# Optimization experiments

Measured on AMD Instinct MI355X. Metric: run time of the kernel, lower is better.

## Reference

```python
import jax, jax.numpy as jnp
import numpy as np
from math import gamma, comb

D_POLY = 4
OFFSET = 2
EVAL_MAX = 1.4
N_NODES = 50000
N_EDGES = 800000
IN_FEATS = 256
H_FEATS = 64
NEG_SLOPE = 0.01  # F.leaky_relu / nn.LeakyReLU default


def _beta(a, b):
    return gamma(a) * gamma(b) / gamma(a + b)


def _calculate_theta2(d=D_POLY):
    # Closed-form expansion of sympy poly in calculate_theta2:
    # f(x) = (x/e)^i * (1 - x/e)^(d-i+offset) / (e * Beta(i+1, d+1-i+offset))
    # Returns ascending-order coefficient lists (theta[k] = coeff of x^k).
    e = EVAL_MAX
    thetas = []
    for i in range(OFFSET, d + 1 + OFFSET):
        m = d - i + OFFSET
        B = _beta(i + 1, d + 1 - i + OFFSET)
        c = np.zeros(d + 1 + OFFSET, dtype=np.float64)
        for j in range(m + 1):
            c[i + j] = (1.0 / e) ** i * comb(m, j) * (-1.0 / e) ** j / (e * B)
        thetas.append([float(v) for v in c])
    return thetas


THETAS = _calculate_theta2()


def setup_inputs() -> dict:
    key = jax.random.key(0)
    k1, k2, k3, k4, k5 = jax.random.split(key, 5)
    x = jax.random.normal(k1, (N_NODES, IN_FEATS), dtype=jnp.float32)
    W = jax.random.normal(k2, (IN_FEATS, H_FEATS), dtype=jnp.float32) * 0.05
    b = jax.random.normal(k3, (H_FEATS,), dtype=jnp.float32) * 0.05
    src = jax.random.randint(k4, (N_EDGES,), 0, N_NODES, dtype=jnp.int32)
    dst = jax.random.randint(k5, (N_EDGES,), 0, N_NODES, dtype=jnp.int32)
    return {"x": x, "W": W, "b": b, "src": src, "dst": dst}


def reference(x, W, b, src, dst):
    # BWGNN forward: linear + LeakyReLU, then 5 Beta-wavelet PolyConv filters.
    h = jax.nn.leaky_relu(x @ W + b, NEG_SLOPE)  # [N, H]
    # out_degrees, clamped to 1, then D^{-1/2}
    deg = jax.ops.segment_sum(jnp.ones_like(src, dtype=h.dtype), src, num_segments=N_NODES)
    d_inv = jnp.clip(deg, 1.0) ** -0.5
    d_inv = d_inv[:, None]  # [N, 1]
    outs = []
    for theta in THETAS:
        f = h
        acc = theta[0] * h
        for k in range(1, len(theta)):
            # unnLaplacian: f <- f - D^{-1/2} A^T D^{-1/2} f  (copy_u/sum SpMM)
            msg = jax.ops.segment_sum((f * d_inv)[src], dst, num_segments=N_NODES)
            f = f - msg * d_inv
            acc = acc + theta[k] * f
        outs.append(acc)
    return jnp.concatenate(outs, axis=1)  # [N, 5*H]
```

## Files before the change

### kernel.cpp

```cpp
#include <hip/hip_runtime.h>
#include <math.h>

#define NN 50000
#define NNH 25000
#define NE 800000
#define INF 256
#define HF 64
#define OUTF 320
#define NB ((NN + 255) / 256)
#define G 128
#define SL (NE / G)

typedef _Float16 half8 __attribute__((ext_vector_type(8)));
typedef float floatx4 __attribute__((ext_vector_type(4)));

static __device__ __forceinline__ unsigned short f2h(float x) {
    _Float16 h = (_Float16)x;
    return *(unsigned short*)&h;
}
static __device__ __forceinline__ float h2f(unsigned short u) {
    _Float16 h = *(_Float16*)&u;
    return (float)h;
}

struct ThetaM { float m[5][7]; };

static void compute_theta(ThetaM& tm) {
    const double e = 1.4;
    auto fact = [](int n) { double r = 1.0; for (int i = 2; i <= n; ++i) r *= i; return r; };
    for (int t = 0; t < 5; ++t) {
        int i = t + 2;
        int mm = 6 - i;
        double B = fact(i) * fact(6 - i) / fact(7);
        for (int k = 0; k < 7; ++k) tm.m[t][k] = 0.f;
        for (int j = 0; j <= mm; ++j) {
            double cb = fact(mm) / (fact(j) * fact(mm - j));
            double v = pow(1.0 / e, (double)i) * cb * pow(-1.0 / e, (double)j) / (e * B);
            tm.m[t][i + j] = (float)v;
        }
    }
}

__global__ __launch_bounds__(1024) void hist_kernel(const int* __restrict__ src,
                                                    const int* __restrict__ dst,
                                                    unsigned short* __restrict__ hist_src,
                                                    unsigned short* __restrict__ hist_dst) {
    __shared__ unsigned int h[NNH];
    int b = blockIdx.x;
    const int* arr = (b < G) ? dst : src;
    unsigned short* outp = (b < G) ? hist_dst : hist_src;
    int bb = (b < G) ? b : b - G;
    for (int i = threadIdx.x; i < NNH; i += 1024) h[i] = 0u;
    __syncthreads();
    int base = bb * SL;
    for (int i = threadIdx.x; i < SL; i += 1024) {
        int d = arr[base + i];
        atomicAdd(&h[d >> 1], 1u << ((d & 1) * 16));
    }
    __syncthreads();
    unsigned int* out32 = (unsigned int*)(outp + (size_t)bb * NN);
    for (int i = threadIdx.x; i < NNH; i += 1024) out32[i] = h[i];
}

__global__ __launch_bounds__(256) void merge_dst_kernel(unsigned short* __restrict__ hist,
                                                        int* __restrict__ cnt,
                                                        int* __restrict__ partial) {
    __shared__ int s[256];
    int tid = threadIdx.x;
    int d = blockIdx.x * 256 + tid;
    int run = 0;
    if (d < NN) {
        for (int b = 0; b < G; ++b) {
            size_t idx = (size_t)b * NN + d;
            int v = hist[idx];
            hist[idx] = (unsigned short)run;
            run += v;
        }
        cnt[d] = run;
    }
    s[tid] = run;
    __syncthreads();
    for (int off = 128; off > 0; off >>= 1) {
        if (tid < off) s[tid] += s[tid + off];
        __syncthreads();
    }
    if (tid == 0) partial[blockIdx.x] = s[0];
}

__global__ __launch_bounds__(256) void merge_src_kernel(const unsigned short* __restrict__ hist,
                                                        float* __restrict__ dinv) {
    int d = blockIdx.x * 256 + threadIdx.x;
    if (d >= NN) return;
    int run = 0;
    for (int b = 0; b < G; ++b) run += hist[(size_t)b * NN + d];
    float dd = (float)run;
    if (dd < 1.f) dd = 1.f;
    dinv[d] = 1.0f / sqrtf(dd);
}

__global__ __launch_bounds__(256) void scan_partials_kernel(const int* __restrict__ partial,
                                                            int* __restrict__ offsets,
                                                            int* __restrict__ row_ptr) {
    __shared__ int s[256];
    int tid = threadIdx.x;
    s[tid] = (tid < NB) ? partial[tid] : 0;
    __syncthreads();
    for (int off = 1; off < 256; off <<= 1) {
        int t = (tid >= off) ? s[tid - off] : 0;
        __syncthreads();
        s[tid] += t;
        __syncthreads();
    }
    if (tid < NB) offsets[tid] = (tid == 0) ? 0 : s[tid - 1];
    if (tid == 0) row_ptr[NN] = NE;
}

__global__ __launch_bounds__(256) void scan_write_kernel(const int* __restrict__ cnt,
                                                         const int* __restrict__ offsets,
                                                         int* __restrict__ row_ptr) {
    __shared__ int s[256];
    int tid = threadIdx.x;
    int gid = blockIdx.x * 256 + tid;
    int c = (gid < NN) ? cnt[gid] : 0;
    s[tid] = c;
    __syncthreads();
    for (int off = 1; off < 256; off <<= 1) {
        int t = (tid >= off) ? s[tid - off] : 0;
        __syncthreads();
        s[tid] += t;
        __syncthreads();
    }
    if (gid < NN) row_ptr[gid] = offsets[blockIdx.x] + s[tid] - c;
}

__global__ __launch_bounds__(1024) void fill_kernel(const int* __restrict__ src,
                                                    const int* __restrict__ dst,
                                                    const unsigned short* __restrict__ hist_dst,
                                                    const int* __restrict__ row_ptr,
                                                    int* __restrict__ col) {
    __shared__ unsigned int cur[NNH];
    int b = blockIdx.x;
    for (int i = threadIdx.x; i < NNH; i += 1024) cur[i] = 0u;
    __syncthreads();
    int base = b * SL;
    const unsigned short* hrow = hist_dst + (size_t)b * NN;
    for (int i = threadIdx.x; i < SL; i += 1024) {
        int d = dst[base + i];
        int sh = (d & 1) * 16;
        unsigned int old = atomicAdd(&cur[d >> 1], 1u << sh);
        int rank = (int)((old >> sh) & 0xFFFFu);
        int pos = row_ptr[d] + (int)hrow[d] + rank;
        col[pos] = src[base + i];
    }
}

__global__ __launch_bounds__(256) void wprep_kernel(const float* __restrict__ W,
                                                    unsigned short* __restrict__ Wt) {
    int id = blockIdx.x * 256 + threadIdx.x;
    if (id >= HF * INF) return;
    int n = id >> 8;
    int k = id & 255;
    Wt[id] = f2h(W[k * HF + n]);
}

__global__ __launch_bounds__(256) void gemm_kernel(const float* __restrict__ x,
                                                   const unsigned short* __restrict__ Wt,
                                                   const float* __restrict__ b,
                                                   const float* __restrict__ dinv,
                                                   float* __restrict__ f,
                                                   unsigned short* __restrict__ g) {
    __shared__ _Float16 wls[64 * 264];
    __shared__ _Float16 xls[64 * 136];
    int tid = threadIdx.x;
    int row0 = blockIdx.x * 64;
    int wave = tid >> 6;
    int lane = tid & 63;
    int q = lane >> 4;
    int ln = lane & 15;

    {
        const uint4* wg = (const uint4*)Wt;
        for (int i = 0; i < 8; ++i) {
            int l = tid + i * 256;
            int r = l >> 5, c = l & 31;
            *(uint4*)&wls[r * 264 + c * 8] = wg[l];
        }
    }

    floatx4 acc[4] = {{0.f,0.f,0.f,0.f},{0.f,0.f,0.f,0.f},{0.f,0.f,0.f,0.f},{0.f,0.f,0.f,0.f}};

    for (int ch = 0; ch < 2; ++ch) {
        __syncthreads();
        for (int i = 0; i < 8; ++i) {
            int l = tid + i * 256;
            int r = l >> 5, c4 = (l & 31) * 4;
            int grow = row0 + r;
            float4 v = make_float4(0.f, 0.f, 0.f, 0.f);
            if (grow < NN) v = *(const float4*)&x[(size_t)grow * INF + ch * 128 + c4];
            ushort4 hv;
            hv.x = f2h(v.x); hv.y = f2h(v.y); hv.z = f2h(v.z); hv.w = f2h(v.w);
            *(ushort4*)&xls[r * 136 + c4] = hv;
        }
        __syncthreads();
        int m = wave * 16 + ln;
        #pragma unroll
        for (int kb4 = 0; kb4 < 4; ++kb4) {
            int kb = kb4 * 32;
            half8 a = *(const half8*)&xls[m * 136 + kb + q * 8];
            int kg = ch * 128 + kb + q * 8;
            #pragma unroll
            for (int t = 0; t < 4; ++t) {
                half8 bb = *(const half8*)&wls[(t * 16 + ln) * 264 + kg];
                acc[t] = __builtin_amdgcn_mfma_f32_16x16x32_f16(a, bb, acc[t], 0, 0, 0);
            }
        }
    }

    float bias[4];
    #pragma unroll
    for (int t = 0; t < 4; ++t) bias[t] = b[t * 16 + ln];
    #pragma unroll
    for (int r = 0; r < 4; ++r) {
        int grow = row0 + wave * 16 + q * 4 + r;
        if (grow < NN) {
            float dv = dinv[grow];
            #pragma unroll
            for (int t = 0; t < 4; ++t) {
                float h = acc[t][r] + bias[t];
                h = (h > 0.f) ? h : 0.01f * h;
                int cidx = t * 16 + ln;
                f[(size_t)grow * HF + cidx] = h;
                g[(size_t)grow * HF + cidx] = f2h(h * dv);
            }
        }
    }
}

__global__ __launch_bounds__(256) void prop_kernel(const int* __restrict__ row_ptr,
                                                   const int* __restrict__ col,
                                                   const float* __restrict__ dinv,
                                                   const unsigned int* __restrict__ g_in,
                                                   const float* __restrict__ f_in, int fin_stride,
                                                   float* __restrict__ f_out, int fout_stride,
                                                   unsigned int* __restrict__ g_out) {
    int gidx = blockIdx.x * 256 + threadIdx.x;
    int wid = gidx >> 5;
    int c2 = threadIdx.x & 31;
    if (wid >= NN) return;
    int start = row_ptr[wid];
    int end   = row_ptr[wid + 1];
    float s0 = 0.f, s1 = 0.f;
    int j = start;
    for (; j + 8 <= end; j += 8) {
        unsigned int u0 = g_in[col[j + 0] * 32 + c2];
        unsigned int u1 = g_in[col[j + 1] * 32 + c2];
        unsigned int u2 = g_in[col[j + 2] * 32 + c2];
        unsigned int u3 = g_in[col[j + 3] * 32 + c2];
        unsigned int u4 = g_in[col[j + 4] * 32 + c2];
        unsigned int u5 = g_in[col[j + 5] * 32 + c2];
        unsigned int u6 = g_in[col[j + 6] * 32 + c2];
        unsigned int u7 = g_in[col[j + 7] * 32 + c2];
        s0 += ((h2f(u0 & 0xFFFF) + h2f(u1 & 0xFFFF)) + (h2f(u2 & 0xFFFF) + h2f(u3 & 0xFFFF)))
            + ((h2f(u4 & 0xFFFF) + h2f(u5 & 0xFFFF)) + (h2f(u6 & 0xFFFF) + h2f(u7 & 0xFFFF)));
        s1 += ((h2f(u0 >> 16) + h2f(u1 >> 16)) + (h2f(u2 >> 16) + h2f(u3 >> 16)))
            + ((h2f(u4 >> 16) + h2f(u5 >> 16)) + (h2f(u6 >> 16) + h2f(u7 >> 16)));
    }
    for (; j < end; ++j) {
        unsigned int u = g_in[col[j] * 32 + c2];
        s0 += h2f(u & 0xFFFF);
        s1 += h2f(u >> 16);
    }
    float dv = dinv[wid];
    float2 fv = *(const float2*)&f_in[(size_t)wid * fin_stride + 2 * c2];
    float fx = fv.x - s0 * dv;
    float fy = fv.y - s1 * dv;
    *(float2*)&f_out[(size_t)wid * fout_stride + 2 * c2] = make_float2(fx, fy);
    if (g_out) g_out[wid * 32 + c2] = (unsigned int)f2h(fx * dv) | ((unsigned int)f2h(fy * dv) << 16);
}

__global__ __launch_bounds__(256) void final_kernel(float* __restrict__ out, ThetaM tm) {
    int idx = blockIdx.x * 256 + threadIdx.x;
    if (idx >= NN * HF) return;
    int n = idx >> 6;
    int c = idx & 63;
    float v[5];
    #pragma unroll
    for (int j = 0; j < 5; ++j) v[j] = out[(size_t)n * OUTF + j * HF + c];
    #pragma unroll
    for (int t = 0; t < 5; ++t) {
        float o = 0.f;
        #pragma unroll
        for (int j = 0; j < 5; ++j) {
            if (j >= t) o += tm.m[t][j + 2] * v[j];
        }
        out[(size_t)n * OUTF + t * HF + c] = o;
    }
}

extern "C" void kernel_launch(void* const* d_in, const int* in_sizes, int n_in,
                              void* d_out, int out_size, void* d_ws, size_t ws_size,
                              hipStream_t stream) {
    const float* x  = (const float*)d_in[0];
    const float* W  = (const float*)d_in[1];
    const float* b  = (const float*)d_in[2];
    const int* src  = (const int*)d_in[3];
    const int* dst  = (const int*)d_in[4];
    float* out = (float*)d_out;

    char* ws = (char*)d_ws;
    size_t off = 0;
    auto alloc = [&](size_t bytes) -> void* {
        void* p = ws + off;
        off += (bytes + 255) & ~(size_t)255;
        return p;
    };
    unsigned short* hist_dst = (unsigned short*)alloc((size_t)G * NN * 2);
    unsigned short* hist_src = (unsigned short*)alloc((size_t)G * NN * 2);
    int*   cnt_dst = (int*)alloc((size_t)NN * 4);
    int*   row_ptr = (int*)alloc((size_t)(NN + 1) * 4);
    int*   partial = (int*)alloc((size_t)NB * 4);
    int*   offsets = (int*)alloc((size_t)NB * 4);
    float* dinv    = (float*)alloc((size_t)NN * 4);
    int*   col     = (int*)alloc((size_t)NE * 4);
    unsigned short* wt = (unsigned short*)alloc((size_t)HF * INF * 2);
    float* fbuf    = (float*)alloc((size_t)NN * HF * 4);
    unsigned short* gA = (unsigned short*)alloc((size_t)NN * HF * 2);
    unsigned short* gB = (unsigned short*)alloc((size_t)NN * HF * 2);

    hist_kernel<<<2 * G, 1024, 0, stream>>>(src, dst, hist_src, hist_dst);
    merge_dst_kernel<<<NB, 256, 0, stream>>>(hist_dst, cnt_dst, partial);
    merge_src_kernel<<<NB, 256, 0, stream>>>(hist_src, dinv);
    scan_partials_kernel<<<1, 256, 0, stream>>>(partial, offsets, row_ptr);
    scan_write_kernel<<<NB, 256, 0, stream>>>(cnt_dst, offsets, row_ptr);
    fill_kernel<<<G, 1024, 0, stream>>>(src, dst, hist_dst, row_ptr, col);
    wprep_kernel<<<(HF * INF + 255) / 256, 256, 0, stream>>>(W, wt);
    gemm_kernel<<<(NN + 63) / 64, 256, 0, stream>>>(x, wt, b, dinv, fbuf, gA);

    const int PB = (NN * 32 + 255) / 256;
    prop_kernel<<<PB, 256, 0, stream>>>(row_ptr, col, dinv, (unsigned int*)gA, fbuf, HF, fbuf, HF, (unsigned int*)gB);
    prop_kernel<<<PB, 256, 0, stream>>>(row_ptr, col, dinv, (unsigned int*)gB, fbuf, HF, out + 0 * HF, OUTF, (unsigned int*)gA);
    prop_kernel<<<PB, 256, 0, stream>>>(row_ptr, col, dinv, (unsigned int*)gA, out + 0 * HF, OUTF, out + 1 * HF, OUTF, (unsigned int*)gB);
    prop_kernel<<<PB, 256, 0, stream>>>(row_ptr, col, dinv, (unsigned int*)gB, out + 1 * HF, OUTF, out + 2 * HF, OUTF, (unsigned int*)gA);
    prop_kernel<<<PB, 256, 0, stream>>>(row_ptr, col, dinv, (unsigned int*)gA, out + 2 * HF, OUTF, out + 3 * HF, OUTF, (unsigned int*)gB);
    prop_kernel<<<PB, 256, 0, stream>>>(row_ptr, col, dinv, (unsigned int*)gB, out + 3 * HF, OUTF, out + 4 * HF, OUTF, nullptr);

    ThetaM tm;
    compute_theta(tm);
    final_kernel<<<(NN * HF + 255) / 256, 256, 0, stream>>>(out, tm);
}
```

Baseline: 346.2 us.

## Pad CSR rows to multiples of four, pack histograms into bytes, use atomic degrees

Destination histograms are packed as 8-bit counts, four nodes per word, which halves shared-memory and workspace traffic. Source degrees are now counted with global atomics instead of a second histogram pass, and the separate source-merge kernel is removed. Each CSR row is padded to a multiple of four with a dummy zero-feature node, so the propagation kernel can load column indices as int4 vectors and needs no scalar tail loop. Nontemporal loads and stores are added to streaming accesses, and the final theta-combine kernel is vectorized over pairs of features. The risks are 8-bit count overflow if any node receives more than 255 edges within one slice, and extra gathers for the padding entries.

```diff
diff --git a/kernel.cpp b/kernel.cpp
--- a/kernel.cpp
+++ b/kernel.cpp
@@ -2,17 +2,19 @@
 #include <math.h>
 
 #define NN 50000
-#define NNH 25000
+#define NN4 12500
 #define NE 800000
 #define INF 256
 #define HF 64
 #define OUTF 320
-#define NB ((NN + 255) / 256)
+#define NB4 ((NN4 + 255) / 256)
 #define G 128
 #define SL (NE / G)
 
 typedef _Float16 half8 __attribute__((ext_vector_type(8)));
 typedef float floatx4 __attribute__((ext_vector_type(4)));
+typedef float f32x2 __attribute__((ext_vector_type(2)));
+typedef float f32x4 __attribute__((ext_vector_type(4)));
 
 static __device__ __forceinline__ unsigned short f2h(float x) {
     _Float16 h = (_Float16)x;
@@ -41,61 +43,73 @@
     }
 }
 
-__global__ __launch_bounds__(1024) void hist_kernel(const int* __restrict__ src,
-                                                    const int* __restrict__ dst,
-                                                    unsigned short* __restrict__ hist_src,
-                                                    unsigned short* __restrict__ hist_dst) {
-    __shared__ unsigned int h[NNH];
+__global__ __launch_bounds__(1024) void zero_kernel(int* __restrict__ deg,
+                                                    unsigned int* __restrict__ gA,
+                                                    unsigned int* __restrict__ gB) {
+    int i = blockIdx.x * 1024 + threadIdx.x;
+    if (i < NN) deg[i] = 0;
+    if (blockIdx.x == 0 && threadIdx.x < 32) {
+        gA[NN * 32 + threadIdx.x] = 0u;
+        gB[NN * 32 + threadIdx.x] = 0u;
+    }
+}
+
+__global__ __launch_bounds__(1024) void histdeg_kernel(const int* __restrict__ src,
+                                                       const int* __restrict__ dst,
+                                                       unsigned int* __restrict__ hist,
+                                                       int* __restrict__ deg) {
+    __shared__ unsigned int h[NN4];
     int b = blockIdx.x;
-    const int* arr = (b < G) ? dst : src;
-    unsigned short* outp = (b < G) ? hist_dst : hist_src;
-    int bb = (b < G) ? b : b - G;
-    for (int i = threadIdx.x; i < NNH; i += 1024) h[i] = 0u;
-    __syncthreads();
-    int base = bb * SL;
+    for (int i = threadIdx.x; i < NN4; i += 1024) h[i] = 0u;
+    __syncthreads();
+    int base = b * SL;
     for (int i = threadIdx.x; i < SL; i += 1024) {
-        int d = arr[base + i];
-        atomicAdd(&h[d >> 1], 1u << ((d & 1) * 16));
-    }
-    __syncthreads();
-    unsigned int* out32 = (unsigned int*)(outp + (size_t)bb * NN);
-    for (int i = threadIdx.x; i < NNH; i += 1024) out32[i] = h[i];
-}
-
-__global__ __launch_bounds__(256) void merge_dst_kernel(unsigned short* __restrict__ hist,
+        int d = dst[base + i];
+        atomicAdd(&h[d >> 2], 1u << ((d & 3) * 8));
+    }
+    for (int i = threadIdx.x; i < SL; i += 1024) {
+        atomicAdd(&deg[src[base + i]], 1);
+    }
+    __syncthreads();
+    unsigned int* out32 = hist + (size_t)b * NN4;
+    for (int i = threadIdx.x; i < NN4; i += 1024) out32[i] = h[i];
+}
+
+__global__ __launch_bounds__(256) void merge_dst_kernel(unsigned int* __restrict__ hist,
+                                                        const int* __restrict__ deg,
                                                         int* __restrict__ cnt,
+                                                        float* __restrict__ dinv,
                                                         int* __restrict__ partial) {
     __shared__ int s[256];
     int tid = threadIdx.x;
-    int d = blockIdx.x * 256 + tid;
-    int run = 0;
-    if (d < NN) {
+    int t = blockIdx.x * 256 + tid;
+    int run0 = 0, run1 = 0, run2 = 0, run3 = 0;
+    if (t < NN4) {
         for (int b = 0; b < G; ++b) {
-            size_t idx = (size_t)b * NN + d;
-            int v = hist[idx];
-            hist[idx] = (unsigned short)run;
-            run += v;
-        }
-        cnt[d] = run;
-    }
-    s[tid] = run;
+            size_t idx = (size_t)b * NN4 + t;
+            unsigned int u = hist[idx];
+            hist[idx] = (unsigned int)run0 | ((unsigned int)run1 << 8) |
+                        ((unsigned int)run2 << 16) | ((unsigned int)run3 << 24);
+            run0 += u & 255u; run1 += (u >> 8) & 255u;
+            run2 += (u >> 16) & 255u; run3 += u >> 24;
+        }
+        *(int4*)&cnt[4 * t] = make_int4(run0, run1, run2, run3);
+        int4 dg = *(const int4*)&deg[4 * t];
+        float d0 = (float)(dg.x < 1 ? 1 : dg.x);
+        float d1 = (float)(dg.y < 1 ? 1 : dg.y);
+        float d2 = (float)(dg.z < 1 ? 1 : dg.z);
+        float d3 = (float)(dg.w < 1 ? 1 : dg.w);
+        *(float4*)&dinv[4 * t] = make_float4(1.0f / sqrtf(d0), 1.0f / sqrtf(d1),
+                                             1.0f / sqrtf(d2), 1.0f / sqrtf(d3));
+    }
+    int pad = ((run0 + 3) & ~3) + ((run1 + 3) & ~3) + ((run2 + 3) & ~3) + ((run3 + 3) & ~3);
+    s[tid] = pad;
     __syncthreads();
     for (int off = 128; off > 0; off >>= 1) {
         if (tid < off) s[tid] += s[tid + off];
         __syncthreads();
     }
     if (tid == 0) partial[blockIdx.x] = s[0];
-}
-
-__global__ __launch_bounds__(256) void merge_src_kernel(const unsigned short* __restrict__ hist,
-                                                        float* __restrict__ dinv) {
-    int d = blockIdx.x * 256 + threadIdx.x;
-    if (d >= NN) return;
-    int run = 0;
-    for (int b = 0; b < G; ++b) run += hist[(size_t)b * NN + d];
-    float dd = (float)run;
-    if (dd < 1.f) dd = 1.f;
-    dinv[d] = 1.0f / sqrtf(dd);
 }
 
 __global__ __launch_bounds__(256) void scan_partials_kernel(const int* __restrict__ partial,
@@ -103,7 +117,7 @@
                                                             int* __restrict__ row_ptr) {
     __shared__ int s[256];
     int tid = threadIdx.x;
-    s[tid] = (tid < NB) ? partial[tid] : 0;
+    s[tid] = (tid < NB4) ? partial[tid] : 0;
     __syncthreads();
     for (int off = 1; off < 256; off <<= 1) {
         int t = (tid >= off) ? s[tid - off] : 0;
@@ -111,44 +125,56 @@
         s[tid] += t;
         __syncthreads();
     }
-    if (tid < NB) offsets[tid] = (tid == 0) ? 0 : s[tid - 1];
-    if (tid == 0) row_ptr[NN] = NE;
+    if (tid < NB4) offsets[tid] = (tid == 0) ? 0 : s[tid - 1];
+    if (tid == NB4 - 1) row_ptr[NN] = s[tid];
 }
 
 __global__ __launch_bounds__(256) void scan_write_kernel(const int* __restrict__ cnt,
                                                          const int* __restrict__ offsets,
-                                                         int* __restrict__ row_ptr) {
+                                                         int* __restrict__ row_ptr,
+                                                         int* __restrict__ col) {
     __shared__ int s[256];
     int tid = threadIdx.x;
-    int gid = blockIdx.x * 256 + tid;
-    int c = (gid < NN) ? cnt[gid] : 0;
-    s[tid] = c;
+    int t = blockIdx.x * 256 + tid;
+    int4 c = make_int4(0, 0, 0, 0);
+    if (t < NN4) c = *(const int4*)&cnt[4 * t];
+    int p0 = (c.x + 3) & ~3, p1 = (c.y + 3) & ~3, p2 = (c.z + 3) & ~3, p3 = (c.w + 3) & ~3;
+    int csum = p0 + p1 + p2 + p3;
+    s[tid] = csum;
     __syncthreads();
     for (int off = 1; off < 256; off <<= 1) {
-        int t = (tid >= off) ? s[tid - off] : 0;
-        __syncthreads();
-        s[tid] += t;
-        __syncthreads();
-    }
-    if (gid < NN) row_ptr[gid] = offsets[blockIdx.x] + s[tid] - c;
+        int v = (tid >= off) ? s[tid - off] : 0;
+        __syncthreads();
+        s[tid] += v;
+        __syncthreads();
+    }
+    if (t < NN4) {
+        int b0 = offsets[blockIdx.x] + s[tid] - csum;
+        int b1 = b0 + p0, b2 = b1 + p1, b3 = b2 + p2;
+        *(int4*)&row_ptr[4 * t] = make_int4(b0, b1, b2, b3);
+        for (int k = c.x; k < p0; ++k) col[b0 + k] = NN;
+        for (int k = c.y; k < p1; ++k) col[b1 + k] = NN;
+        for (int k = c.z; k < p2; ++k) col[b2 + k] = NN;
+        for (int k = c.w; k < p3; ++k) col[b3 + k] = NN;
+    }
 }
 
 __global__ __launch_bounds__(1024) void fill_kernel(const int* __restrict__ src,
                                                     const int* __restrict__ dst,
-                                                    const unsigned short* __restrict__ hist_dst,
+                                                    const unsigned char* __restrict__ hist8,
                                                     const int* __restrict__ row_ptr,
                                                     int* __restrict__ col) {
-    __shared__ unsigned int cur[NNH];
+    __shared__ unsigned int cur[NN4];
     int b = blockIdx.x;
-    for (int i = threadIdx.x; i < NNH; i += 1024) cur[i] = 0u;
+    for (int i = threadIdx.x; i < NN4; i += 1024) cur[i] = 0u;
     __syncthreads();
     int base = b * SL;
-    const unsigned short* hrow = hist_dst + (size_t)b * NN;
+    const unsigned char* hrow = hist8 + (size_t)b * NN;
     for (int i = threadIdx.x; i < SL; i += 1024) {
         int d = dst[base + i];
-        int sh = (d & 1) * 16;
-        unsigned int old = atomicAdd(&cur[d >> 1], 1u << sh);
-        int rank = (int)((old >> sh) & 0xFFFFu);
+        int sh = (d & 3) * 8;
+        unsigned int old = atomicAdd(&cur[d >> 2], 1u << sh);
+        int rank = (int)((old >> sh) & 255u);
         int pos = row_ptr[d] + (int)hrow[d] + rank;
         col[pos] = src[base + i];
     }
@@ -195,10 +221,10 @@
             int l = tid + i * 256;
             int r = l >> 5, c4 = (l & 31) * 4;
             int grow = row0 + r;
-            float4 v = make_float4(0.f, 0.f, 0.f, 0.f);
-            if (grow < NN) v = *(const float4*)&x[(size_t)grow * INF + ch * 128 + c4];
+            f32x4 v = {0.f, 0.f, 0.f, 0.f};
+            if (grow < NN) v = __builtin_nontemporal_load((const f32x4*)&x[(size_t)grow * INF + ch * 128 + c4]);
             ushort4 hv;
-            hv.x = f2h(v.x); hv.y = f2h(v.y); hv.z = f2h(v.z); hv.w = f2h(v.w);
+            hv.x = f2h(v[0]); hv.y = f2h(v[1]); hv.z = f2h(v[2]); hv.w = f2h(v[3]);
             *(ushort4*)&xls[r * 136 + c4] = hv;
         }
         __syncthreads();
@@ -247,53 +273,60 @@
     int wid = gidx >> 5;
     int c2 = threadIdx.x & 31;
     if (wid >= NN) return;
-    int start = row_ptr[wid];
-    int end   = row_ptr[wid + 1];
+    int j   = row_ptr[wid];
+    int end = row_ptr[wid + 1];
     float s0 = 0.f, s1 = 0.f;
-    int j = start;
     for (; j + 8 <= end; j += 8) {
-        unsigned int u0 = g_in[col[j + 0] * 32 + c2];
-        unsigned int u1 = g_in[col[j + 1] * 32 + c2];
-        unsigned int u2 = g_in[col[j + 2] * 32 + c2];
-        unsigned int u3 = g_in[col[j + 3] * 32 + c2];
-        unsigned int u4 = g_in[col[j + 4] * 32 + c2];
-        unsigned int u5 = g_in[col[j + 5] * 32 + c2];
-        unsigned int u6 = g_in[col[j + 6] * 32 + c2];
-        unsigned int u7 = g_in[col[j + 7] * 32 + c2];
+        int4 ca = *(const int4*)&col[j];
+        int4 cb = *(const int4*)&col[j + 4];
+        unsigned int u0 = g_in[ca.x * 32 + c2];
+        unsigned int u1 = g_in[ca.y * 32 + c2];
+        unsigned int u2 = g_in[ca.z * 32 + c2];
+        unsigned int u3 = g_in[ca.w * 32 + c2];
+        unsigned int u4 = g_in[cb.x * 32 + c2];
+        unsigned int u5 = g_in[cb.y * 32 + c2];
+        unsigned int u6 = g_in[cb.z * 32 + c2];
+        unsigned int u7 = g_in[cb.w * 32 + c2];
         s0 += ((h2f(u0 & 0xFFFF) + h2f(u1 & 0xFFFF)) + (h2f(u2 & 0xFFFF) + h2f(u3 & 0xFFFF)))
             + ((h2f(u4 & 0xFFFF) + h2f(u5 & 0xFFFF)) + (h2f(u6 & 0xFFFF) + h2f(u7 & 0xFFFF)));
         s1 += ((h2f(u0 >> 16) + h2f(u1 >> 16)) + (h2f(u2 >> 16) + h2f(u3 >> 16)))
             + ((h2f(u4 >> 16) + h2f(u5 >> 16)) + (h2f(u6 >> 16) + h2f(u7 >> 16)));
     }
-    for (; j < end; ++j) {
-        unsigned int u = g_in[col[j] * 32 + c2];
-        s0 += h2f(u & 0xFFFF);
-        s1 += h2f(u >> 16);
+    if (j < end) {
+        int4 ca = *(const int4*)&col[j];
+        unsigned int u0 = g_in[ca.x * 32 + c2];
+        unsigned int u1 = g_in[ca.y * 32 + c2];
+        unsigned int u2 = g_in[ca.z * 32 + c2];
+        unsigned int u3 = g_in[ca.w * 32 + c2];
+        s0 += (h2f(u0 & 0xFFFF) + h2f(u1 & 0xFFFF)) + (h2f(u2 & 0xFFFF) + h2f(u3 & 0xFFFF));
+        s1 += (h2f(u0 >> 16) + h2f(u1 >> 16)) + (h2f(u2 >> 16) + h2f(u3 >> 16));
     }
     float dv = dinv[wid];
-    float2 fv = *(const float2*)&f_in[(size_t)wid * fin_stride + 2 * c2];
-    float fx = fv.x - s0 * dv;
-    float fy = fv.y - s1 * dv;
-    *(float2*)&f_out[(size_t)wid * fout_stride + 2 * c2] = make_float2(fx, fy);
+    f32x2 fv = __builtin_nontemporal_load((const f32x2*)&f_in[(size_t)wid * fin_stride + 2 * c2]);
+    float fx = fv[0] - s0 * dv;
+    float fy = fv[1] - s1 * dv;
+    f32x2 ov; ov[0] = fx; ov[1] = fy;
+    __builtin_nontemporal_store(ov, (f32x2*)&f_out[(size_t)wid * fout_stride + 2 * c2]);
     if (g_out) g_out[wid * 32 + c2] = (unsigned int)f2h(fx * dv) | ((unsigned int)f2h(fy * dv) << 16);
 }
 
 __global__ __launch_bounds__(256) void final_kernel(float* __restrict__ out, ThetaM tm) {
     int idx = blockIdx.x * 256 + threadIdx.x;
-    if (idx >= NN * HF) return;
-    int n = idx >> 6;
-    int c = idx & 63;
-    float v[5];
+    if (idx >= NN * 32) return;
+    int n = idx >> 5;
+    int c = (idx & 31) * 2;
+    f32x2 v[5];
     #pragma unroll
-    for (int j = 0; j < 5; ++j) v[j] = out[(size_t)n * OUTF + j * HF + c];
+    for (int j = 0; j < 5; ++j)
+        v[j] = __builtin_nontemporal_load((const f32x2*)&out[(size_t)n * OUTF + j * HF + c]);
     #pragma unroll
     for (int t = 0; t < 5; ++t) {
-        float o = 0.f;
+        f32x2 o = {0.f, 0.f};
         #pragma unroll
         for (int j = 0; j < 5; ++j) {
-            if (j >= t) o += tm.m[t][j + 2] * v[j];
-        }
-        out[(size_t)n * OUTF + t * HF + c] = o;
+            if (j >= t) { o[0] += tm.m[t][j + 2] * v[j][0]; o[1] += tm.m[t][j + 2] * v[j][1]; }
+        }
+        __builtin_nontemporal_store(o, (f32x2*)&out[(size_t)n * OUTF + t * HF + c]);
     }
 }
 
@@ -314,25 +347,25 @@
         off += (bytes + 255) & ~(size_t)255;
         return p;
     };
-    unsigned short* hist_dst = (unsigned short*)alloc((size_t)G * NN * 2);
-    unsigned short* hist_src = (unsigned short*)alloc((size_t)G * NN * 2);
-    int*   cnt_dst = (int*)alloc((size_t)NN * 4);
+    unsigned int* hist_dst = (unsigned int*)alloc((size_t)G * NN4 * 4);
+    int*   deg     = (int*)alloc((size_t)NN * 4);
+    int*   cnt     = (int*)alloc((size_t)NN * 4);
     int*   row_ptr = (int*)alloc((size_t)(NN + 1) * 4);
-    int*   partial = (int*)alloc((size_t)NB * 4);
-    int*   offsets = (int*)alloc((size_t)NB * 4);
+    int*   partial = (int*)alloc((size_t)NB4 * 4);
+    int*   offsets = (int*)alloc((size_t)NB4 * 4);
     float* dinv    = (float*)alloc((size_t)NN * 4);
-    int*   col     = (int*)alloc((size_t)NE * 4);
+    int*   col     = (int*)alloc((size_t)(NE + 4 * NN) * 4);
     unsigned short* wt = (unsigned short*)alloc((size_t)HF * INF * 2);
     float* fbuf    = (float*)alloc((size_t)NN * HF * 4);
-    unsigned short* gA = (unsigned short*)alloc((size_t)NN * HF * 2);
-    unsigned short* gB = (unsigned short*)alloc((size_t)NN * HF * 2);
-
-    hist_kernel<<<2 * G, 1024, 0, stream>>>(src, dst, hist_src, hist_dst);
-    merge_dst_kernel<<<NB, 256, 0, stream>>>(hist_dst, cnt_dst, partial);
-    merge_src_kernel<<<NB, 256, 0, stream>>>(hist_src, dinv);
+    unsigned short* gA = (unsigned short*)alloc((size_t)(NN + 1) * HF * 2);
+    unsigned short* gB = (unsigned short*)alloc((size_t)(NN + 1) * HF * 2);
+
+    zero_kernel<<<(NN + 1023) / 1024, 1024, 0, stream>>>(deg, (unsigned int*)gA, (unsigned int*)gB);
+    histdeg_kernel<<<G, 1024, 0, stream>>>(src, dst, hist_dst, deg);
+    merge_dst_kernel<<<NB4, 256, 0, stream>>>(hist_dst, deg, cnt, dinv, partial);
     scan_partials_kernel<<<1, 256, 0, stream>>>(partial, offsets, row_ptr);
-    scan_write_kernel<<<NB, 256, 0, stream>>>(cnt_dst, offsets, row_ptr);
-    fill_kernel<<<G, 1024, 0, stream>>>(src, dst, hist_dst, row_ptr, col);
+    scan_write_kernel<<<NB4, 256, 0, stream>>>(cnt, offsets, row_ptr, col);
+    fill_kernel<<<G, 1024, 0, stream>>>(src, dst, (const unsigned char*)hist_dst, row_ptr, col);
     wprep_kernel<<<(HF * INF + 255) / 256, 256, 0, stream>>>(W, wt);
     gemm_kernel<<<(NN + 63) / 64, 256, 0, stream>>>(x, wt, b, dinv, fbuf, gA);
 
@@ -346,5 +379,5 @@
 
     ThetaM tm;
     compute_theta(tm);
-    final_kernel<<<(NN * HF + 255) / 256, 256, 0, stream>>>(out, tm);
-}
+    final_kernel<<<(NN * 32 + 255) / 256, 256, 0, stream>>>(out, tm);
+}
```

Measured after the change: 357.2 us. 3.2% more time.
